# Performance work log

Hardware: AMD Instinct MI355X
Metric: run time of the kernel (lower is better)

Reference implementation:

```python
import jax, jax.numpy as jnp
import numpy as np

PS = 16          # patch_size
E = 256          # embed_dim
NH = 4           # num_heads
THR = 1.5        # entropy_threshold (bits)
LN_EPS = 1e-5


def _ln(x, g, b):
    m = x.mean(-1, keepdims=True)
    v = ((x - m) ** 2).mean(-1, keepdims=True)
    return (x - m) / jnp.sqrt(v + LN_EPS) * g + b


def _forward(video, conv_w, conv_b, wq_w, wq_b, wk_w, wk_b, wv_w, wv_b,
             lnq_g, lnq_b, lnk_g, lnk_b, lnv_g, lnv_b,
             in_proj_w, in_proj_b, out_proj_w, out_proj_b,
             dense_w, dense_b, bproj_w, bproj_b, group_query, ent_table):
    # Conv3d(3->E, k=(3,PS,PS), s=(2,PS,PS), p=(1,0,0)) + ReLU
    x = jax.lax.conv_general_dilated(
        video, conv_w, window_strides=(2, PS, PS),
        padding=((1, 1), (0, 0), (0, 0)),
        dimension_numbers=('NCDHW', 'OIDHW', 'NCDHW'))
    x = jax.nn.relu(x + conv_b[None, :, None, None, None])
    B = x.shape[0]
    tokens = x.reshape(B, E, -1).transpose(0, 2, 1)  # [B, N, E]
    N = tokens.shape[1]

    # per-token byte (no_grad in torch)
    byte = jax.lax.stop_gradient(
        jnp.clip(jnp.round(tokens.mean(-1) * 255.0), 0, 255)).astype(jnp.int32)  # [B, N]
    # entropy predictor: probs = softmax(ent_table[last_byte]) (last byte of running seq)
    logits = ent_table[byte[0]]                      # [N, 256]
    p = jax.nn.softmax(logits, axis=-1)
    ent = -(p * jnp.log2(p + 1e-9)).sum(-1)          # [N]
    boundary = (ent > THR).astype(jnp.int32)
    seg = jnp.cumsum(boundary) - boundary            # exclusive cumsum -> segment id per token

    # DecoderCrossAttention with a single shared group_query per segment
    q0 = jnp.broadcast_to(group_query, (B, 1, E))    # byte_representations
    query = _ln(q0 @ wq_w.T + wq_b, lnq_g, lnq_b)    # [B,1,E]
    k = _ln(tokens @ wk_w.T + wk_b, lnk_g, lnk_b)    # [B,N,E]
    v = _ln(tokens @ wv_w.T + wv_b, lnv_g, lnv_b)

    Wqi, Wki, Wvi = in_proj_w[:E], in_proj_w[E:2 * E], in_proj_w[2 * E:]
    bqi, bki, bvi = in_proj_b[:E], in_proj_b[E:2 * E], in_proj_b[2 * E:]
    dh = E // NH
    qp = ((query @ Wqi.T + bqi) * (dh ** -0.5)).reshape(B, NH, dh)  # [B,H,dh]
    kp = (k @ Wki.T + bki).reshape(B, N, NH, dh)
    vp = (v @ Wvi.T + bvi).reshape(B, N, NH, dh)

    scores = jnp.einsum('bhd,bnhd->nbh', qp, kp)     # [N,B,H]
    smax = jax.ops.segment_max(scores, seg, num_segments=N)   # [N,B,H]
    w = jnp.exp(scores - smax[seg])
    denom = jax.ops.segment_sum(w, seg, num_segments=N)       # [N,B,H]
    num = jax.ops.segment_sum(w[..., None] * vp.transpose(1, 0, 2, 3),
                              seg, num_segments=N)            # [N,B,H,dh]
    count = jax.ops.segment_sum(jnp.ones((N,), scores.dtype), seg, num_segments=N)
    valid = count > 0
    safe = jnp.where(valid[:, None, None], denom, 1.0)
    attn = (num / safe[..., None]).transpose(1, 0, 2, 3).reshape(B, N, E)
    out = attn @ out_proj_w.T + out_proj_b
    out = out @ dense_w.T + dense_b
    out = out + q0                                   # residual with byte_representations
    patches = out @ bproj_w.T + bproj_b              # binary_proj
    return jnp.where(valid[None, :, None], patches, 0.0)  # [B, N, E] padded


def setup_inputs() -> dict:
    key = jax.random.key(0)
    ks = jax.random.split(key, 16)
    rn = lambda k, s, sc=0.02: jax.random.normal(k, s, jnp.float32) * sc
    z = lambda *s: jnp.zeros(s, jnp.float32)
    o = lambda *s: jnp.ones(s, jnp.float32)
    return {
        'video': jax.random.normal(ks[0], (4, 3, 32, 224, 224), jnp.float32),
        'conv_w': rn(ks[1], (E, 3, 3, PS, PS)), 'conv_b': z(E),
        'wq_w': rn(ks[2], (E, E)), 'wq_b': z(E),
        'wk_w': rn(ks[3], (E, E)), 'wk_b': z(E),
        'wv_w': rn(ks[4], (E, E)), 'wv_b': z(E),
        'lnq_g': o(E), 'lnq_b': z(E),
        'lnk_g': o(E), 'lnk_b': z(E),
        'lnv_g': o(E), 'lnv_b': z(E),
        'in_proj_w': rn(ks[5], (3 * E, E)), 'in_proj_b': z(3 * E),
        'out_proj_w': rn(ks[6], (E, E)), 'out_proj_b': z(E),
        'dense_w': rn(ks[7], (E, E)), 'dense_b': z(E),
        'bproj_w': rn(ks[8], (E, E)), 'bproj_b': z(E),
        'group_query': jax.random.normal(ks[9], (1, 1, E), jnp.float32),
        'ent_table': jax.random.normal(ks[10], (256, 256), jnp.float32) * 6.0,
    }


def reference(video, conv_w, conv_b, wq_w, wq_b, wk_w, wk_b, wv_w, wv_b,
              lnq_g, lnq_b, lnk_g, lnk_b, lnv_g, lnv_b,
              in_proj_w, in_proj_b, out_proj_w, out_proj_b,
              dense_w, dense_b, bproj_w, bproj_b, group_query, ent_table):
    return _forward(video, conv_w, conv_b, wq_w, wq_b, wk_w, wk_b, wv_w, wv_b,
                    lnq_g, lnq_b, lnk_g, lnk_b, lnv_g, lnv_b,
                    in_proj_w, in_proj_b, out_proj_w, out_proj_b,
                    dense_w, dense_b, bproj_w, bproj_b, group_query, ent_table)
```

## Files before the change

### kernel.cpp

```cpp
#include <hip/hip_runtime.h>
#include <hip/hip_bf16.h>
#include <math.h>

#define NTOK 3136
#define MT 12544
#define KCV 2304
#define THRESH 1.5f
#define LN_EPS 1e-5f

typedef short short8 __attribute__((ext_vector_type(8)));
typedef float f32x4 __attribute__((ext_vector_type(4)));

__device__ __forceinline__ unsigned short f2bf(float f) {
    unsigned int u = __float_as_uint(f);
    u += 0x7fffu + ((u >> 16) & 1u);
    return (unsigned short)(u >> 16);
}
__device__ __forceinline__ float bf2f(unsigned short h) {
    return __uint_as_float(((unsigned int)h) << 16);
}
__device__ __forceinline__ unsigned int cvt_pk_bf16(float x0, float x1) {
    union { __hip_bfloat162 h; unsigned int u; } cv;
    cv.h = __float22bfloat162_rn(make_float2(x0, x1));
    return cv.u;
}
__device__ __forceinline__ void async16(const void* g, void* l) {
    __builtin_amdgcn_global_load_lds((const __attribute__((address_space(1))) void*)g,
                                     (__attribute__((address_space(3))) void*)l, 16, 0, 0);
}

__device__ __forceinline__ float wsum(float v) {
#pragma unroll
    for (int o = 32; o > 0; o >>= 1) v += __shfl_xor(v, o);
    return v;
}
__device__ __forceinline__ float wmax(float v) {
#pragma unroll
    for (int o = 32; o > 0; o >>= 1) v = fmaxf(v, __shfl_xor(v, o));
    return v;
}

__global__ __launch_bounds__(256) void prep_k(
    const float* __restrict__ cw, unsigned short* __restrict__ cwh,
    unsigned short* __restrict__ cwl,
    const float* __restrict__ s0, const float* __restrict__ s1, const float* __restrict__ s2,
    unsigned short* __restrict__ dst,
    const float* __restrict__ gq, const float* __restrict__ wq_w,
    const float* __restrict__ wq_b, const float* __restrict__ lnq_g,
    const float* __restrict__ lnq_b, const float* __restrict__ inW,
    const float* __restrict__ inB, float* __restrict__ qp,
    const float* __restrict__ Wd, const float* __restrict__ Wo,
    const float* __restrict__ bo, const float* __restrict__ bd,
    float* __restrict__ D1, float* __restrict__ tvec)
{
    const int blk = blockIdx.x;
    const int t = threadIdx.x;
    if (blk < 288) {
        int i = blk * 256 + t;
        int e = i & 255, kg = i >> 8;
        const float4* sp = (const float4*)(cw + (size_t)e * KCV + kg * 8);
        float4 x0 = sp[0], x1 = sp[1];
        float av[8] = {x0.x, x0.y, x0.z, x0.w, x1.x, x1.y, x1.z, x1.w};
        short8 hh, ll;
#pragma unroll
        for (int j = 0; j < 8; ++j) {
            unsigned short h = f2bf(av[j]);
            hh[j] = (short)h;
            ll[j] = (short)f2bf(av[j] - bf2f(h));
        }
        size_t off = (size_t)kg * 2048 + e * 8;
        *(short8*)&cwh[off] = hh;
        *(short8*)&cwl[off] = ll;
    } else if (blk < 1568) {
        int i = (blk - 288) * 256 + t;
        if (i >= 327680) return;
        float v;
        if      (i <  65536) v = s0[i];
        else if (i < 131072) v = s1[i - 65536];
        else                 v = s2[i - 131072];
        dst[i] = f2bf(v);
    } else if (blk == 1568) {
        __shared__ float sh[256];
        __shared__ float red[256];
        float acc = wq_b[t];
        for (int j = 0; j < 256; j++) acc += gq[j] * wq_w[t * 256 + j];
        red[t] = acc; __syncthreads();
        for (int o = 128; o > 0; o >>= 1) { if (t < o) red[t] += red[t + o]; __syncthreads(); }
        float m = red[0] * (1.f / 256.f);
        __syncthreads();
        float d = acc - m;
        red[t] = d * d; __syncthreads();
        for (int o = 128; o > 0; o >>= 1) { if (t < o) red[t] += red[t + o]; __syncthreads(); }
        float inv = 1.f / sqrtf(red[0] * (1.f / 256.f) + LN_EPS);
        sh[t] = d * inv * lnq_g[t] + lnq_b[t];
        __syncthreads();
        float a2 = inB[t];
        for (int j = 0; j < 256; j++) a2 += sh[j] * inW[t * 256 + j];
        qp[t] = a2 * 0.125f;
    } else if (blk < 1825) {
        int i = blk - 1569;
        float acc = 0.f;
        for (int k = 0; k < 256; k++) acc += Wd[i * 256 + k] * Wo[k * 256 + t];
        D1[i * 256 + t] = acc;
    } else {
        float acc = bd[t] + gq[t];
        for (int k = 0; k < 256; k++) acc += Wd[t * 256 + k] * bo[k];
        tvec[t] = acc;
    }
}

__global__ __launch_bounds__(256) void conv_mfma_k(
    const float* __restrict__ video, const unsigned short* __restrict__ cwh,
    const unsigned short* __restrict__ cwl, const float* __restrict__ cbias,
    float* __restrict__ tokmean4, unsigned short* __restrict__ outB,
    const float* __restrict__ Wb, const float* __restrict__ D1,
    const float* __restrict__ tvec, const float* __restrict__ bb,
    unsigned short* __restrict__ WcB, float* __restrict__ bc)
{
    __shared__ __align__(16) unsigned short Bh[8192], Bl[8192];
    const int t    = threadIdx.x;
    if (blockIdx.x >= 784) {
        const int pblk = blockIdx.x - 784;
        if (pblk < 256) {
            float acc = 0.f;
            for (int k = 0; k < 256; k++) acc += Wb[pblk * 256 + k] * D1[k * 256 + t];
            WcB[pblk * 256 + t] = f2bf(acc);
        } else {
            float acc = bb[t];
            for (int k = 0; k < 256; k++) acc += Wb[t * 256 + k] * tvec[k];
            bc[t] = acc;
        }
        return;
    }
    const int lane = t & 63;
    const int w    = t >> 6;
    const int l15  = lane & 15, lq = lane >> 4;
    const int v_  = blockIdx.x;
    const int s_  = (v_ & 7) * 98 + (v_ >> 3);
    const int mb  = s_ >> 2, eb = s_ & 3;
    const int m0  = mb * 64, e0 = eb * 64;

    const int m = m0 + w * 16 + l15;
    const int b = m / NTOK, n = m % NTOK;
    const int d = n / 196, hw = n % 196;
    const int h = hw / 14, ww = hw % 14;
    const float* vb = video + (size_t)(b * 3) * (32 * 50176) + (h * 16) * 224 + ww * 16;
    const int dbase = 2 * d - 1;

    f32x4 acc[4] = {};
    float4 a0, a1, a2, a3, b0, b1, b2, b3;
    short8 rh0, rh1, rl0, rl1;

#define BLOAD(s)                                                                     \
    {                                                                                \
        const size_t g0 = (size_t)((s) * 8 + w) * 2048 + (e0 + lane) * 8;            \
        const size_t g1 = g0 + 4 * 2048;                                             \
        rh0 = *(const short8*)(cwh + g0);                                            \
        rh1 = *(const short8*)(cwh + g1);                                            \
        rl0 = *(const short8*)(cwl + g0);                                            \
        rl1 = *(const short8*)(cwl + g1);                                            \
    }
#define BSTORE(buf)                                                                  \
    {                                                                                \
        const int o = (buf) * 4096 + w * 512 + lane * 8;                             \
        *(short8*)&Bh[o]        = rh0;                                               \
        *(short8*)&Bh[o + 2048] = rh1;                                               \
        *(short8*)&Bl[o]        = rl0;                                               \
        *(short8*)&Bl[o + 2048] = rl1;                                               \
    }
#define LOAD_A32(k0v, x0, x1)                                                        \
    {                                                                                \
        const int k0  = (k0v) + lq * 8;                                              \
        const int c   = k0 / 768;                                                    \
        const int rem = k0 - c * 768;                                                \
        const int kd  = rem >> 8;                                                    \
        const int r2  = rem & 255;                                                   \
        const int id  = dbase + kd;                                                  \
        x0 = make_float4(0.f, 0.f, 0.f, 0.f); x1 = x0;                               \
        if (id >= 0) {                                                               \
            const float* p = vb + (size_t)c * (32 * 50176) + id * 50176 +            \
                             (r2 >> 4) * 224 + (r2 & 15);                            \
            x0 = *(const float4*)p;                                                  \
            x1 = *(const float4*)(p + 4);                                            \
        }                                                                            \
    }
#define CVT_AB(y0, y1, fah, fal)                                                     \
    short8 fah, fal;                                                                 \
    {                                                                                \
        float av[8] = {y0.x, y0.y, y0.z, y0.w, y1.x, y1.y, y1.z, y1.w};              \
        unsigned int ph[4], pl[4];                                                   \
        _Pragma("unroll")                                                            \
        for (int j = 0; j < 4; ++j) {                                                \
            float u0 = av[2 * j], u1 = av[2 * j + 1];                                \
            unsigned int hu = cvt_pk_bf16(u0, u1);                                   \
            float r0 = u0 - __uint_as_float(hu << 16);                               \
            float r1 = u1 - __uint_as_float(hu & 0xffff0000u);                       \
            ph[j] = hu;                                                              \
            pl[j] = cvt_pk_bf16(r0, r1);                                             \
        }                                                                            \
        int4 phv = make_int4(ph[0], ph[1], ph[2], ph[3]);                            \
        int4 plv = make_int4(pl[0], pl[1], pl[2], pl[3]);                            \
        fah = *(short8*)&phv;                                                        \
        fal = *(short8*)&plv;                                                        \
    }

    BLOAD(0);
    LOAD_A32(0, a0, a1);
    LOAD_A32(32, a2, a3);
    BSTORE(0);
    __syncthreads();

    for (int s = 0; s < 36; ++s) {
        const int cbuf = s & 1;
        if (s + 1 < 36) {
            BLOAD(s + 1);
            LOAD_A32((s + 1) * 64,      b0, b1);
            LOAD_A32((s + 1) * 64 + 32, b2, b3);
        }
        {
            CVT_AB(a0, a1, fah, fal);
            const int rb = cbuf * 4096 + lq * 512 + l15 * 8;
#pragma unroll
            for (int ct = 0; ct < 4; ++ct) {
                short8 fbh = *(const short8*)&Bh[rb + ct * 128];
                short8 fbl = *(const short8*)&Bl[rb + ct * 128];
                acc[ct] = __builtin_amdgcn_mfma_f32_16x16x32_bf16(fah, fbh, acc[ct], 0, 0, 0);
                acc[ct] = __builtin_amdgcn_mfma_f32_16x16x32_bf16(fah, fbl, acc[ct], 0, 0, 0);
                acc[ct] = __builtin_amdgcn_mfma_f32_16x16x32_bf16(fal, fbh, acc[ct], 0, 0, 0);
            }
        }
        {
            CVT_AB(a2, a3, fah, fal);
            const int rb = cbuf * 4096 + (4 + lq) * 512 + l15 * 8;
#pragma unroll
            for (int ct = 0; ct < 4; ++ct) {
                short8 fbh = *(const short8*)&Bh[rb + ct * 128];
                short8 fbl = *(const short8*)&Bl[rb + ct * 128];
                acc[ct] = __builtin_amdgcn_mfma_f32_16x16x32_bf16(fah, fbh, acc[ct], 0, 0, 0);
                acc[ct] = __builtin_amdgcn_mfma_f32_16x16x32_bf16(fah, fbl, acc[ct], 0, 0, 0);
                acc[ct] = __builtin_amdgcn_mfma_f32_16x16x32_bf16(fal, fbh, acc[ct], 0, 0, 0);
            }
        }
        if (s + 1 < 36) BSTORE(cbuf ^ 1);
        __syncthreads();
        a0 = b0; a1 = b1; a2 = b2; a3 = b3;
    }
#undef BLOAD
#undef BSTORE
#undef LOAD_A32
#undef CVT_AB

    const int rbase = m0 + w * 16 + lq * 4;
    float rsum[4] = {0.f, 0.f, 0.f, 0.f};
#pragma unroll
    for (int ct = 0; ct < 4; ++ct) {
        int e = e0 + ct * 16 + l15;
        float bias = cbias[e];
#pragma unroll
        for (int r = 0; r < 4; ++r) {
            float vv = fmaxf(acc[ct][r] + bias, 0.f);
            outB[(size_t)(rbase + r) * 256 + e] = f2bf(vv);
            rsum[r] += vv;
        }
    }
    if (m0 < NTOK) {
#pragma unroll
        for (int r = 0; r < 4; ++r) {
            float sv = rsum[r];
            sv += __shfl_xor(sv, 1); sv += __shfl_xor(sv, 2);
            sv += __shfl_xor(sv, 4); sv += __shfl_xor(sv, 8);
            if (l15 == 0) tokmean4[(size_t)eb * NTOK + rbase + r] = sv;
        }
    }
}

__global__ __launch_bounds__(256) void gemm_single_k(
    const unsigned short* __restrict__ A, const unsigned short* __restrict__ W,
    const float* __restrict__ bias, const float* __restrict__ addvec,
    const int* __restrict__ Sptr, float* __restrict__ outF, unsigned short* __restrict__ outB)
{
    __shared__ __align__(16) unsigned short As[8192], Bs[8192];
    const int t = threadIdx.x, lane = t & 63, w = t >> 6;
    const int v_ = blockIdx.x;
    const int s_ = (v_ & 7) * 98 + (v_ >> 3);
    const int m0 = (s_ >> 2) * 64, e0 = (s_ & 3) * 64;
    const int l15 = lane & 15, lq = lane >> 4;
    const unsigned short* ga = A + (size_t)(m0 + lane) * 256;
    const unsigned short* gb = W + (size_t)(e0 + lane) * 256;
#pragma unroll
    for (int kg = w; kg < 16; kg += 4) {
        async16(ga + kg * 8, &As[kg * 512]);
        async16(gb + kg * 8, &Bs[kg * 512]);
    }
    f32x4 acc[4] = {};
    __syncthreads();
#pragma unroll
    for (int s = 0; s < 4; ++s) {
        int kg = s * 4 + lq;
        short8 a = *(const short8*)&As[kg * 512 + (w * 16 + l15) * 8];
#pragma unroll
        for (int ct = 0; ct < 4; ++ct) {
            short8 bb = *(const short8*)&Bs[kg * 512 + (ct * 16 + l15) * 8];
            acc[ct] = __builtin_amdgcn_mfma_f32_16x16x32_bf16(a, bb, acc[ct], 0, 0, 0);
        }
    }
    __syncthreads();
#pragma unroll
    for (int kg = w; kg < 16; kg += 4) {
        async16(ga + (16 + kg) * 8, &As[kg * 512]);
        async16(gb + (16 + kg) * 8, &Bs[kg * 512]);
    }
    __syncthreads();
#pragma unroll
    for (int s = 0; s < 4; ++s) {
        int kg = s * 4 + lq;
        short8 a = *(const short8*)&As[kg * 512 + (w * 16 + l15) * 8];
#pragma unroll
        for (int ct = 0; ct < 4; ++ct) {
            short8 bb = *(const short8*)&Bs[kg * 512 + (ct * 16 + l15) * 8];
            acc[ct] = __builtin_amdgcn_mfma_f32_16x16x32_bf16(a, bb, acc[ct], 0, 0, 0);
        }
    }
    int S = Sptr ? *Sptr : 0x7fffffff;
    int rbase = m0 + w * 16 + lq * 4;
#pragma unroll
    for (int ct = 0; ct < 4; ++ct) {
        int e = e0 + ct * 16 + l15;
        float bv = bias[e] + (addvec ? addvec[e] : 0.f);
#pragma unroll
        for (int r = 0; r < 4; ++r) {
            int mm = rbase + r;
            float vv = acc[ct][r] + bv;
            if ((mm % NTOK) >= S) vv = 0.f;
            size_t off = (size_t)mm * 256 + e;
            if (outF) outF[off] = vv;
            if (outB) outB[off] = f2bf(vv);
        }
    }
}

__global__ __launch_bounds__(256) void gemm_dual_k(
    const unsigned short* __restrict__ A0, const unsigned short* __restrict__ A1,
    const unsigned short* __restrict__ W,
    const float* __restrict__ bias0, const float* __restrict__ bias1,
    unsigned short* __restrict__ outB0, unsigned short* __restrict__ outB1,
    const float* __restrict__ tokmean4, const float* __restrict__ ent_table,
    int* __restrict__ boundary)
{
    __shared__ __align__(16) unsigned short As[8192], Bs[8192];
    const int t = threadIdx.x, lane = t & 63, w = t >> 6;
    if (blockIdx.x >= 1568) {
        int n = (blockIdx.x - 1568) * 4 + w;
        float s0 = tokmean4[n];
        float s1 = tokmean4[NTOK + n];
        float s2 = tokmean4[2 * NTOK + n];
        float s3 = tokmean4[3 * NTOK + n];
        float mean = ((s0 + s1) + (s2 + s3)) * (1.f / 256.f);
        float bf = rintf(mean * 255.f);
        bf = fminf(fmaxf(bf, 0.f), 255.f);
        int byte = (int)bf;
        const float4 lg = reinterpret_cast<const float4*>(ent_table + byte * 256)[lane];
        float mx = wmax(fmaxf(fmaxf(lg.x, lg.y), fmaxf(lg.z, lg.w)));
        float e0 = expf(lg.x - mx), e1 = expf(lg.y - mx);
        float e2 = expf(lg.z - mx), e3 = expf(lg.w - mx);
        float z = wsum(e0 + e1 + e2 + e3);
        float iz = 1.f / z;
        float p0 = e0 * iz, p1 = e1 * iz, p2 = e2 * iz, p3 = e3 * iz;
        float ep = -(p0 * log2f(p0 + 1e-9f) + p1 * log2f(p1 + 1e-9f) +
                     p2 * log2f(p2 + 1e-9f) + p3 * log2f(p3 + 1e-9f));
        ep = wsum(ep);
        if (lane == 0) boundary[n] = (ep > THRESH) ? 1 : 0;
        return;
    }
    const int v_ = blockIdx.x;
    const int s_ = (v_ & 7) * 196 + (v_ >> 3);
    const int mb = s_ >> 3, ebg = s_ & 7;
    const int half = ebg >> 2;
    const unsigned short* A = half ? A1 : A0;
    const float* bias = half ? bias1 : bias0;
    unsigned short* outB = half ? outB1 : outB0;
    const int m0 = mb * 64, eg0 = ebg * 64, el0 = (ebg & 3) * 64;
    const int l15 = lane & 15, lq = lane >> 4;
    const unsigned short* ga = A + (size_t)(m0 + lane) * 256;
    const unsigned short* gb = W + (size_t)(eg0 + lane) * 256;
#pragma unroll
    for (int kg = w; kg < 16; kg += 4) {
        async16(ga + kg * 8, &As[kg * 512]);
        async16(gb + kg * 8, &Bs[kg * 512]);
    }
    f32x4 acc[4] = {};
    __syncthreads();
#pragma unroll
    for (int s = 0; s < 4; ++s) {
        int kg = s * 4 + lq;
        short8 a = *(const short8*)&As[kg * 512 + (w * 16 + l15) * 8];
#pragma unroll
        for (int ct = 0; ct < 4; ++ct) {
            short8 bb = *(const short8*)&Bs[kg * 512 + (ct * 16 + l15) * 8];
            acc[ct] = __builtin_amdgcn_mfma_f32_16x16x32_bf16(a, bb, acc[ct], 0, 0, 0);
        }
    }
    __syncthreads();
#pragma unroll
    for (int kg = w; kg < 16; kg += 4) {
        async16(ga + (16 + kg) * 8, &As[kg * 512]);
        async16(gb + (16 + kg) * 8, &Bs[kg * 512]);
    }
    __syncthreads();
#pragma unroll
    for (int s = 0; s < 4; ++s) {
        int kg = s * 4 + lq;
        short8 a = *(const short8*)&As[kg * 512 + (w * 16 + l15) * 8];
#pragma unroll
        for (int ct = 0; ct < 4; ++ct) {
            short8 bb = *(const short8*)&Bs[kg * 512 + (ct * 16 + l15) * 8];
            acc[ct] = __builtin_amdgcn_mfma_f32_16x16x32_bf16(a, bb, acc[ct], 0, 0, 0);
        }
    }
    int rbase = m0 + w * 16 + lq * 4;
#pragma unroll
    for (int ct = 0; ct < 4; ++ct) {
        int e = el0 + ct * 16 + l15;
        float bv = bias[e];
#pragma unroll
        for (int r = 0; r < 4; ++r) {
            float vv = acc[ct][r] + bv;
            outB[(size_t)(rbase + r) * 256 + e] = f2bf(vv);
        }
    }
}

__global__ __launch_bounds__(256, 2) void gemm_ln_k(
    const unsigned short* __restrict__ A0, const unsigned short* __restrict__ A1,
    const unsigned short* __restrict__ W,
    const float* __restrict__ bias0, const float* __restrict__ bias1,
    const float* __restrict__ g0, const float* __restrict__ b0,
    const float* __restrict__ g1, const float* __restrict__ b1,
    unsigned short* __restrict__ outVp, const float* __restrict__ qp,
    float* __restrict__ sc,
    const int* __restrict__ boundary, int* __restrict__ seg_start, int* __restrict__ Sptr)
{
    __shared__ __align__(16) unsigned short As[16384], Bs[8192];
    __shared__ float pst[2][4][64];
    __shared__ float rmean[64], rinv[64];
    __shared__ int sums[256];
    const int t = threadIdx.x, lane = t & 63, w = t >> 6;
    if (blockIdx.x >= 1568) {
        const int CH = 13;
        int base = t * CH;
        int s = 0;
        for (int i = 0; i < CH; i++) { int n = base + i; if (n < NTOK) s += boundary[n]; }
        sums[t] = s; __syncthreads();
        for (int o = 1; o < 256; o <<= 1) {
            int v = sums[t];
            int u = (t >= o) ? sums[t - o] : 0;
            __syncthreads();
            sums[t] = v + u;
            __syncthreads();
        }
        int run = (t == 0) ? 0 : sums[t - 1];
        if (t == 0) seg_start[0] = 0;
        for (int i = 0; i < CH; i++) {
            int n = base + i;
            if (n >= NTOK) break;
            int v = boundary[n];
            if (n == NTOK - 1) { Sptr[0] = run + 1; seg_start[run + 1] = NTOK; }
            if (v && (n + 1 < NTOK)) seg_start[run + 1] = n + 1;
            run += v;
        }
        return;
    }
    const int v_ = blockIdx.x;
    const int s_ = (v_ & 7) * 196 + (v_ >> 3);
    const int mb = s_ >> 3, ebg = s_ & 7;
    const int half = ebg >> 2;
    const unsigned short* A = half ? A1 : A0;
    const float* bias = half ? bias1 : bias0;
    const float* lng  = half ? g1 : g0;
    const float* lnb  = half ? b1 : b0;
    const int m0 = mb * 64, eg0 = ebg * 64, el0 = (ebg & 3) * 64;
    const int l15 = lane & 15, lq = lane >> 4;
    const unsigned short* ga = A + (size_t)(m0 + lane) * 256;
    const unsigned short* gb = W + (size_t)(eg0 + lane) * 256;
#pragma unroll
    for (int kg = w; kg < 32; kg += 4) async16(ga + kg * 8, &As[kg * 512]);
#pragma unroll
    for (int kg = w; kg < 16; kg += 4) async16(gb + kg * 8, &Bs[kg * 512]);
    __syncthreads();
    {
        float sum = 0.f, sq = 0.f;
#pragma unroll
        for (int k8 = 0; k8 < 8; ++k8) {
            short8 x = *(const short8*)&As[(w * 8 + k8) * 512 + lane * 8];
#pragma unroll
            for (int j = 0; j < 8; ++j) {
                float xv = bf2f((unsigned short)x[j]);
                sum += xv; sq += xv * xv;
            }
        }
        pst[0][w][lane] = sum; pst[1][w][lane] = sq;
    }
    __syncthreads();
    if (w == 0) {
        float s4 = (pst[0][0][lane] + pst[0][1][lane]) + (pst[0][2][lane] + pst[0][3][lane]);
        float q4 = (pst[1][0][lane] + pst[1][1][lane]) + (pst[1][2][lane] + pst[1][3][lane]);
        float mean = s4 * (1.f / 256.f);
        float var  = q4 * (1.f / 256.f) - mean * mean;
        rmean[lane] = mean;
        rinv[lane]  = 1.f / sqrtf(var + LN_EPS);
    }
    __syncthreads();
    const float myMean = rmean[w * 16 + l15];
    const float myInv  = rinv [w * 16 + l15];

    f32x4 acc[4] = {};
#pragma unroll
    for (int ph = 0; ph < 2; ++ph) {
        if (ph == 1) {
            __syncthreads();
#pragma unroll
            for (int kg = w; kg < 16; kg += 4) async16(gb + (16 + kg) * 8, &Bs[kg * 512]);
            __syncthreads();
        }
#pragma unroll
        for (int s = 0; s < 4; ++s) {
            int kg = ph * 16 + s * 4 + lq;
            short8 araw = *(const short8*)&As[kg * 512 + (w * 16 + l15) * 8];
            float4 gA = *(const float4*)&lng[kg * 8];
            float4 gB = *(const float4*)&lng[kg * 8 + 4];
            float4 bA = *(const float4*)&lnb[kg * 8];
            float4 bB = *(const float4*)&lnb[kg * 8 + 4];
            float y[8];
            y[0] = (bf2f((unsigned short)araw[0]) - myMean) * myInv * gA.x + bA.x;
            y[1] = (bf2f((unsigned short)araw[1]) - myMean) * myInv * gA.y + bA.y;
            y[2] = (bf2f((unsigned short)araw[2]) - myMean) * myInv * gA.z + bA.z;
            y[3] = (bf2f((unsigned short)araw[3]) - myMean) * myInv * gA.w + bA.w;
            y[4] = (bf2f((unsigned short)araw[4]) - myMean) * myInv * gB.x + bB.x;
            y[5] = (bf2f((unsigned short)araw[5]) - myMean) * myInv * gB.y + bB.y;
            y[6] = (bf2f((unsigned short)araw[6]) - myMean) * myInv * gB.z + bB.z;
            y[7] = (bf2f((unsigned short)araw[7]) - myMean) * myInv * gB.w + bB.w;
            int4 pk = make_int4(cvt_pk_bf16(y[0], y[1]), cvt_pk_bf16(y[2], y[3]),
                                cvt_pk_bf16(y[4], y[5]), cvt_pk_bf16(y[6], y[7]));
            short8 a = *(short8*)&pk;
            const int bkg = s * 4 + lq;
#pragma unroll
            for (int ct = 0; ct < 4; ++ct) {
                short8 bb = *(const short8*)&Bs[bkg * 512 + (ct * 16 + l15) * 8];
                acc[ct] = __builtin_amdgcn_mfma_f32_16x16x32_bf16(a, bb, acc[ct], 0, 0, 0);
            }
        }
    }
    int rbase = m0 + w * 16 + lq * 4;
    if (half == 0) {
        float sp[4] = {0.f, 0.f, 0.f, 0.f};
#pragma unroll
        for (int ct = 0; ct < 4; ++ct) {
            int e = el0 + ct * 16 + l15;
            float bv = bias[e];
            float qv = qp[e];
#pragma unroll
            for (int r = 0; r < 4; ++r) sp[r] += (acc[ct][r] + bv) * qv;
        }
#pragma unroll
        for (int r = 0; r < 4; ++r) {
            sp[r] += __shfl_xor(sp[r], 1); sp[r] += __shfl_xor(sp[r], 2);
            sp[r] += __shfl_xor(sp[r], 4); sp[r] += __shfl_xor(sp[r], 8);
        }
        if (l15 == 0) {
#pragma unroll
            for (int r = 0; r < 4; ++r) {
                int mm = rbase + r;
                int bb = mm / NTOK, nn = mm % NTOK;
                sc[(bb * 4 + ebg) * NTOK + nn] = sp[r];
            }
        }
    } else {
#pragma unroll
        for (int ct = 0; ct < 4; ++ct) {
            int e = el0 + ct * 16 + l15;
            float bv = bias[e];
#pragma unroll
            for (int r = 0; r < 4; ++r) {
                float vv = acc[ct][r] + bv;
                outVp[(size_t)(rbase + r) * 256 + e] = f2bf(vv);
            }
        }
    }
}

__global__ __launch_bounds__(256) void attn_bf_k(const float* __restrict__ sc,
    const unsigned short* __restrict__ vp, const int* __restrict__ seg_start,
    const int* __restrict__ Sptr, unsigned short* __restrict__ attn)
{
    int b    = blockIdx.y;
    int h    = threadIdx.x >> 6;
    int lane = threadIdx.x & 63;
    int S = *Sptr;
    const unsigned short* vpb0 = vp + (size_t)b * NTOK * 256 + h * 64 + lane;
    for (int s = blockIdx.x; s < S; s += gridDim.x) {
        int st = seg_start[s], en = seg_start[s + 1];
        const float* scr = sc + (b * 4 + h) * NTOK;
        float m = -1e30f;
        for (int n = st; n < en; n++) m = fmaxf(m, scr[n]);
        float den = 0.f, acc = 0.f;
        for (int n = st; n < en; n++) {
            float wgt = expf(scr[n] - m);
            den += wgt;
            acc += wgt * bf2f(vpb0[(size_t)n * 256]);
        }
        attn[((size_t)b * NTOK + s) * 256 + h * 64 + lane] = f2bf(acc / den);
    }
}

extern "C" void kernel_launch(void* const* d_in, const int* in_sizes, int n_in,
                              void* d_out, int out_size, void* d_ws, size_t ws_size,
                              hipStream_t stream)
{
    const float* video      = (const float*)d_in[0];
    const float* conv_w     = (const float*)d_in[1];
    const float* conv_b     = (const float*)d_in[2];
    const float* wq_w       = (const float*)d_in[3];
    const float* wq_b       = (const float*)d_in[4];
    const float* wk_w       = (const float*)d_in[5];
    const float* wk_b       = (const float*)d_in[6];
    const float* wv_w       = (const float*)d_in[7];
    const float* wv_b       = (const float*)d_in[8];
    const float* lnq_g      = (const float*)d_in[9];
    const float* lnq_b      = (const float*)d_in[10];
    const float* lnk_g      = (const float*)d_in[11];
    const float* lnk_b      = (const float*)d_in[12];
    const float* lnv_g      = (const float*)d_in[13];
    const float* lnv_b      = (const float*)d_in[14];
    const float* in_proj_w  = (const float*)d_in[15];
    const float* in_proj_b  = (const float*)d_in[16];
    const float* out_proj_w = (const float*)d_in[17];
    const float* out_proj_b = (const float*)d_in[18];
    const float* dense_w    = (const float*)d_in[19];
    const float* dense_b    = (const float*)d_in[20];
    const float* bproj_w    = (const float*)d_in[21];
    const float* bproj_b    = (const float*)d_in[22];
    const float* group_q    = (const float*)d_in[23];
    const float* ent_table  = (const float*)d_in[24];
    float* out = (float*)d_out;

    float* tokmean4 = (float*)d_ws;
    unsigned short* Pk  = (unsigned short*)(tokmean4 + 16384);
    unsigned short* Pv  = Pk  + (size_t)MT * 256;
    unsigned short* B1  = Pv  + (size_t)MT * 256;
    unsigned short* B3v = B1  + (size_t)MT * 256;
    unsigned short* cwh = B3v + (size_t)MT * 256;
    unsigned short* cwl = cwh + 256 * KCV;
    unsigned short* wpool = cwl + 256 * KCV;
    float* sc = (float*)(wpool + 524288);
    float* qp = sc + 16 * NTOK;
    int* boundary  = (int*)(qp + 256);
    int* seg_start = boundary + NTOK;
    int* Sp        = seg_start + (NTOK + 1);
    float* D1   = (float*)(Sp + 64);
    float* tvec = D1 + 65536;
    float* bc   = tvec + 256;

    const unsigned short* inpb = wpool + 131072;
    unsigned short* WcB        = wpool + 327680;

    dim3 blk(256);
    prep_k<<<dim3(1826), blk, 0, stream>>>(conv_w, cwh, cwl,
                                           wk_w, wv_w, in_proj_w, wpool,
                                           group_q, wq_w, wq_b, lnq_g, lnq_b,
                                           in_proj_w, in_proj_b, qp,
                                           dense_w, out_proj_w, out_proj_b, dense_b,
                                           D1, tvec);
    conv_mfma_k<<<dim3(1041), blk, 0, stream>>>(video, cwh, cwl, conv_b, tokmean4, B1,
                                                bproj_w, D1, tvec, bproj_b, WcB, bc);
    gemm_dual_k<<<dim3(2352), blk, 0, stream>>>(B1, B1, wpool, wk_b, wv_b, Pk, Pv,
                                                tokmean4, ent_table, boundary);
    gemm_ln_k<<<dim3(1569), blk, 0, stream>>>(Pk, Pv, inpb + 65536,
                                              in_proj_b + 256, in_proj_b + 512,
                                              lnk_g, lnk_b, lnv_g, lnv_b,
                                              B3v, qp, sc,
                                              boundary, seg_start, Sp);
    attn_bf_k<<<dim3(512, 4), blk, 0, stream>>>(sc, B3v, seg_start, Sp, B1);
    gemm_single_k<<<dim3(784), blk, 0, stream>>>(B1, WcB, bc,
                                                 nullptr, Sp, out, nullptr);
}
```

Baseline: 300.2 us.

## Fuse segment attention pooling with output projection GEMM in one kernel

```diff
diff --git a/kernel.cpp b/kernel.cpp
--- a/kernel.cpp
+++ b/kernel.cpp
@@ -274,71 +274,6 @@
     }
 }
 
-__global__ __launch_bounds__(256) void gemm_single_k(
-    const unsigned short* __restrict__ A, const unsigned short* __restrict__ W,
-    const float* __restrict__ bias, const float* __restrict__ addvec,
-    const int* __restrict__ Sptr, float* __restrict__ outF, unsigned short* __restrict__ outB)
-{
-    __shared__ __align__(16) unsigned short As[8192], Bs[8192];
-    const int t = threadIdx.x, lane = t & 63, w = t >> 6;
-    const int v_ = blockIdx.x;
-    const int s_ = (v_ & 7) * 98 + (v_ >> 3);
-    const int m0 = (s_ >> 2) * 64, e0 = (s_ & 3) * 64;
-    const int l15 = lane & 15, lq = lane >> 4;
-    const unsigned short* ga = A + (size_t)(m0 + lane) * 256;
-    const unsigned short* gb = W + (size_t)(e0 + lane) * 256;
-#pragma unroll
-    for (int kg = w; kg < 16; kg += 4) {
-        async16(ga + kg * 8, &As[kg * 512]);
-        async16(gb + kg * 8, &Bs[kg * 512]);
-    }
-    f32x4 acc[4] = {};
-    __syncthreads();
-#pragma unroll
-    for (int s = 0; s < 4; ++s) {
-        int kg = s * 4 + lq;
-        short8 a = *(const short8*)&As[kg * 512 + (w * 16 + l15) * 8];
-#pragma unroll
-        for (int ct = 0; ct < 4; ++ct) {
-            short8 bb = *(const short8*)&Bs[kg * 512 + (ct * 16 + l15) * 8];
-            acc[ct] = __builtin_amdgcn_mfma_f32_16x16x32_bf16(a, bb, acc[ct], 0, 0, 0);
-        }
-    }
-    __syncthreads();
-#pragma unroll
-    for (int kg = w; kg < 16; kg += 4) {
-        async16(ga + (16 + kg) * 8, &As[kg * 512]);
-        async16(gb + (16 + kg) * 8, &Bs[kg * 512]);
-    }
-    __syncthreads();
-#pragma unroll
-    for (int s = 0; s < 4; ++s) {
-        int kg = s * 4 + lq;
-        short8 a = *(const short8*)&As[kg * 512 + (w * 16 + l15) * 8];
-#pragma unroll
-        for (int ct = 0; ct < 4; ++ct) {
-            short8 bb = *(const short8*)&Bs[kg * 512 + (ct * 16 + l15) * 8];
-            acc[ct] = __builtin_amdgcn_mfma_f32_16x16x32_bf16(a, bb, acc[ct], 0, 0, 0);
-        }
-    }
-    int S = Sptr ? *Sptr : 0x7fffffff;
-    int rbase = m0 + w * 16 + lq * 4;
-#pragma unroll
-    for (int ct = 0; ct < 4; ++ct) {
-        int e = e0 + ct * 16 + l15;
-        float bv = bias[e] + (addvec ? addvec[e] : 0.f);
-#pragma unroll
-        for (int r = 0; r < 4; ++r) {
-            int mm = rbase + r;
-            float vv = acc[ct][r] + bv;
-            if ((mm % NTOK) >= S) vv = 0.f;
-            size_t off = (size_t)mm * 256 + e;
-            if (outF) outF[off] = vv;
-            if (outB) outB[off] = f2bf(vv);
-        }
-    }
-}
-
 __global__ __launch_bounds__(256) void gemm_dual_k(
     const unsigned short* __restrict__ A0, const unsigned short* __restrict__ A1,
     const unsigned short* __restrict__ W,
@@ -588,27 +523,89 @@
     }
 }
 
-__global__ __launch_bounds__(256) void attn_bf_k(const float* __restrict__ sc,
-    const unsigned short* __restrict__ vp, const int* __restrict__ seg_start,
-    const int* __restrict__ Sptr, unsigned short* __restrict__ attn)
+__global__ __launch_bounds__(256) void attn_proj_k(
+    const float* __restrict__ sc, const unsigned short* __restrict__ vp,
+    const int* __restrict__ seg_start, const int* __restrict__ Sptr,
+    const unsigned short* __restrict__ WcB, const float* __restrict__ bc,
+    float* __restrict__ out)
 {
-    int b    = blockIdx.y;
-    int h    = threadIdx.x >> 6;
-    int lane = threadIdx.x & 63;
-    int S = *Sptr;
-    const unsigned short* vpb0 = vp + (size_t)b * NTOK * 256 + h * 64 + lane;
-    for (int s = blockIdx.x; s < S; s += gridDim.x) {
-        int st = seg_start[s], en = seg_start[s + 1];
+    __shared__ __align__(16) unsigned short As[16384], Bs[8192];
+    const int t = threadIdx.x, lane = t & 63, w = t >> 6;
+    const int m0 = blockIdx.x * 64;
+    const int b  = blockIdx.y;
+    const int l15 = lane & 15, lq = lane >> 4;
+    const int S = *Sptr;
+
+    {
+        const int h = w;
         const float* scr = sc + (b * 4 + h) * NTOK;
-        float m = -1e30f;
-        for (int n = st; n < en; n++) m = fmaxf(m, scr[n]);
-        float den = 0.f, acc = 0.f;
-        for (int n = st; n < en; n++) {
-            float wgt = expf(scr[n] - m);
-            den += wgt;
-            acc += wgt * bf2f(vpb0[(size_t)n * 256]);
-        }
-        attn[((size_t)b * NTOK + s) * 256 + h * 64 + lane] = f2bf(acc / den);
+        const unsigned short* vpb0 = vp + (size_t)b * NTOK * 256 + h * 64 + lane;
+        const int adst = ((h * 8 + (lane >> 3)) * 64) * 8 + (lane & 7);
+        for (int mseg = 0; mseg < 64; ++mseg) {
+            int s = m0 + mseg;
+            unsigned short val = 0;
+            if (s < S) {
+                int st = seg_start[s], en = seg_start[s + 1];
+                float mx = -1e30f;
+                for (int n = st; n < en; n++) mx = fmaxf(mx, scr[n]);
+                float den = 0.f, acc = 0.f;
+                for (int n = st; n < en; n++) {
+                    float wgt = expf(scr[n] - mx);
+                    den += wgt;
+                    acc += wgt * bf2f(vpb0[(size_t)n * 256]);
+                }
+                val = f2bf(acc / den);
+            }
+            As[adst + mseg * 8] = val;
+        }
+    }
+    __syncthreads();
+
+    const int rb_m = w * 16 + lq * 4;
+#pragma unroll 1
+    for (int ec = 0; ec < 4; ++ec) {
+        const unsigned short* gb = WcB + (size_t)(ec * 64 + lane) * 256;
+        f32x4 acc[4] = {};
+#pragma unroll
+        for (int kg = w; kg < 16; kg += 4) async16(gb + kg * 8, &Bs[kg * 512]);
+        __syncthreads();
+#pragma unroll
+        for (int s4 = 0; s4 < 4; ++s4) {
+            int kg = s4 * 4 + lq;
+            short8 a = *(const short8*)&As[kg * 512 + (w * 16 + l15) * 8];
+#pragma unroll
+            for (int ct = 0; ct < 4; ++ct) {
+                short8 bb = *(const short8*)&Bs[kg * 512 + (ct * 16 + l15) * 8];
+                acc[ct] = __builtin_amdgcn_mfma_f32_16x16x32_bf16(a, bb, acc[ct], 0, 0, 0);
+            }
+        }
+        __syncthreads();
+#pragma unroll
+        for (int kg = w; kg < 16; kg += 4) async16(gb + (16 + kg) * 8, &Bs[kg * 512]);
+        __syncthreads();
+#pragma unroll
+        for (int s4 = 0; s4 < 4; ++s4) {
+            int kgg = 16 + s4 * 4 + lq;
+            short8 a = *(const short8*)&As[kgg * 512 + (w * 16 + l15) * 8];
+#pragma unroll
+            for (int ct = 0; ct < 4; ++ct) {
+                short8 bb = *(const short8*)&Bs[(s4 * 4 + lq) * 512 + (ct * 16 + l15) * 8];
+                acc[ct] = __builtin_amdgcn_mfma_f32_16x16x32_bf16(a, bb, acc[ct], 0, 0, 0);
+            }
+        }
+        __syncthreads();
+#pragma unroll
+        for (int ct = 0; ct < 4; ++ct) {
+            int e = ec * 64 + ct * 16 + l15;
+            float bv = bc[e];
+#pragma unroll
+            for (int r = 0; r < 4; ++r) {
+                int s = m0 + rb_m + r;
+                float vv = acc[ct][r] + bv;
+                if (s >= S) vv = 0.f;
+                out[((size_t)b * NTOK + s) * 256 + e] = vv;
+            }
+        }
     }
 }
 
@@ -679,7 +676,5 @@
                                               lnk_g, lnk_b, lnv_g, lnv_b,
                                               B3v, qp, sc,
                                               boundary, seg_start, Sp);
-    attn_bf_k<<<dim3(512, 4), blk, 0, stream>>>(sc, B3v, seg_start, Sp, B1);
-    gemm_single_k<<<dim3(784), blk, 0, stream>>>(B1, WcB, bc,
-                                                 nullptr, Sp, out, nullptr);
-}
+    attn_proj_k<<<dim3(49, 4), blk, 0, stream>>>(sc, B3v, seg_start, Sp, WcB, bc, out);
+}
```

Measured after the change: 354.1 us. 18.0% more time.
